# Optimization experiments

Hardware: AMD Instinct MI355X
Metric: run time of the kernel (lower is better)

## Reference

```python
import jax, jax.numpy as jnp
import numpy as np

N = 1024
H = 4096
W = 4096
K_COUNTS = 10
IOU_T = 0.5
NEG = -1e30  # -inf stand-in for unrecorded groups


def _box_iou(b):
    # b: [N,4] xyxy pixel coords -> [N,N] IoU (torchvision.ops.box_iou)
    area = (b[:, 2] - b[:, 0]) * (b[:, 3] - b[:, 1])
    ix1 = jnp.maximum(b[:, None, 0], b[None, :, 0])
    iy1 = jnp.maximum(b[:, None, 1], b[None, :, 1])
    ix2 = jnp.minimum(b[:, None, 2], b[None, :, 2])
    iy2 = jnp.minimum(b[:, None, 3], b[None, :, 3])
    inter = jnp.clip(ix2 - ix1, 0.0) * jnp.clip(iy2 - iy1, 0.0)
    return inter / (area[:, None] + area[None, :] - inter)


def _c_wsl(iou_gt, scores, counts):
    # Faithful vectorized c_wsl_fast: for every start box i, greedily sweep
    # j = i+1..N-1 adding boxes compatible (IoU <= T) with all current members;
    # when a group hits `counts` at the TOP of a j-iteration it is recorded
    # (check-before-add semantics, so a group completed at j = N-1 is never
    # recorded, matching the original break-based control flow). The final
    # answer is the LAST start achieving the max recorded score (>= update).
    n = scores.shape[0]
    starts = jnp.arange(n)
    carry0 = (
        jnp.eye(n, dtype=bool),            # sel[i, k]: box k in group of start i
        jnp.ones(n, jnp.int32),            # group sizes
        scores,                            # group scores
        jnp.zeros(n, bool),                # recorded flag (== break)
        jnp.full(n, NEG, scores.dtype),    # recorded score
        jnp.zeros((n, n), bool),           # recorded membership
    )

    def step(c, xs):
        j, sj, iou_j = xs  # iou_j = iou_gt[j] (> T bool row; matrix symmetric)
        sel, size, score, rec, rec_score, rec_sel = c
        active = (j > starts) & (~rec)
        do_rec = active & (size == counts)
        rec_sel = jnp.where(do_rec[:, None], sel, rec_sel)
        rec_score = jnp.where(do_rec, score, rec_score)
        rec = rec | do_rec
        compat = ~jnp.any(sel & iou_j[None, :], axis=1)
        add = active & (~do_rec) & (size < counts) & compat
        sel = sel.at[:, j].set(sel[:, j] | add)
        size = size + add.astype(size.dtype)
        score = score + jnp.where(add, sj, jnp.zeros((), score.dtype))
        return (sel, size, score, rec, rec_score, rec_sel), None

    (_, _, _, rec, rec_score, rec_sel), _ = jax.lax.scan(
        step, carry0, (starts, scores, iou_gt))
    masked = jnp.where(rec, rec_score, NEG)
    best = (n - 1) - jnp.argmax(masked[::-1])  # last argmax == '>=' update rule
    return jnp.where(jnp.any(rec), rec_sel[best], jnp.zeros(n, bool))


def reference(bbox, obj_scores, probs, counts):
    Hh, Ww = probs.shape
    # score_bbox_heatmap(reduction='mean'): mean of probs[y1:y2, x1:x2] per box,
    # computed exactly for all boxes with a zero-padded summed-area table.
    sat = jnp.pad(jnp.cumsum(jnp.cumsum(probs, axis=0), axis=1), ((1, 0), (1, 0)))
    x1 = jnp.clip(jnp.floor(bbox[:, 0]).astype(jnp.int32), 0, Ww)
    y1 = jnp.clip(jnp.floor(bbox[:, 1]).astype(jnp.int32), 0, Hh)
    x2 = jnp.clip(jnp.floor(bbox[:, 2]).astype(jnp.int32), 0, Ww)
    y2 = jnp.clip(jnp.floor(bbox[:, 3]).astype(jnp.int32), 0, Hh)
    sums = sat[y2, x2] - sat[y1, x2] - sat[y2, x1] + sat[y1, x1]
    cnt = jnp.maximum((y2 - y1) * (x2 - x1), 1).astype(probs.dtype)
    box_scores = sums / cnt
    # agg_score_method == 'mean'
    scores = 0.5 * (obj_scores + box_scores)
    # sort descending, then greedy IoU grouping on sorted boxes
    order = jnp.argsort(-scores)
    bbox_s = bbox[order]
    scores_s = scores[order]
    iou_gt = _box_iou(bbox_s) > IOU_T
    sel = _c_wsl(iou_gt, scores_s, counts)
    return scores_s * sel.astype(scores_s.dtype)


def setup_inputs() -> dict:
    key = jax.random.key(0)
    k1, k2, k3, k4, k5, k6 = jax.random.split(key, 6)
    cx = jax.random.uniform(k1, (N,), minval=0.15, maxval=0.85) * W
    cy = jax.random.uniform(k2, (N,), minval=0.15, maxval=0.85) * H
    bw = jnp.maximum(jax.random.uniform(k3, (N,), minval=0.02, maxval=0.25) * W, 8.0)
    bh = jnp.maximum(jax.random.uniform(k4, (N,), minval=0.02, maxval=0.25) * H, 8.0)
    bbox = jnp.stack([cx - bw / 2, cy - bh / 2, cx + bw / 2, cy + bh / 2], axis=1)
    obj_scores = jax.random.uniform(k5, (N,))
    probs = jax.random.uniform(k6, (H, W))
    return {"bbox": bbox, "obj_scores": obj_scores, "probs": probs, "counts": K_COUNTS}
```

## Files before the change

### kernel.cpp

```cpp
#include <hip/hip_runtime.h>

#define HH 4096
#define WW 4096
#define NB 1024
#define NCHUNK 256
#define CROWS 16
#define IOU_T 0.5f

typedef unsigned long long u64;

constexpr size_t OFF_PART   = 0;
constexpr size_t OFF_SC64   = OFF_PART   + (size_t)NCHUNK * WW * 8;
constexpr size_t OFF_ORDER  = OFF_SC64   + (size_t)NB * 8;
constexpr size_t OFF_CTR    = OFF_ORDER  + (size_t)NB * 4;
constexpr size_t OFF_IOU    = OFF_CTR    + 64;
constexpr size_t OFF_RECSC  = OFF_IOU    + (size_t)NB * 16 * 8;
constexpr size_t OFF_RECSEL = OFF_RECSC  + (size_t)NB * 8;
constexpr size_t OFF_CC     = OFF_RECSEL + (size_t)NB * 16 * 8;


__global__ void __launch_bounds__(256) k_stage(const float* __restrict__ probs,
        const float* __restrict__ bbox,
        double* __restrict__ part, float* __restrict__ Cc, int* __restrict__ ctr) {
    __shared__ int xlo_s[CROWS], xhi_s[CROWS];
    __shared__ int2 rng_s[CROWS];
    int tid = blockIdx.x * 256 + threadIdx.x;
    int c  = tid >> 10;
    int xq = tid & 1023;
    int t  = threadIdx.x;
    if (blockIdx.x == 0 && t == 0) *ctr = 0;
    if (t < CROWS) { xlo_s[t] = WW + 1; xhi_s[t] = -1; }
    __syncthreads();
    int r0 = c * CROWS;
    for (int i = t; i < NB; i += 256) {
        float4 bb = ((const float4*)bbox)[i];
        int x1 = min(max((int)floorf(bb.x), 0), WW);
        int y1 = min(max((int)floorf(bb.y), 0), HH);
        int x2 = min(max((int)floorf(bb.z), 0), WW);
        int y2 = min(max((int)floorf(bb.w), 0), HH);
        int ra = y1 - 1 - r0, rb = y2 - 1 - r0;
        if (ra >= 0 && ra < CROWS) { atomicMin(&xlo_s[ra], x1); atomicMax(&xhi_s[ra], x2); }
        if (rb >= 0 && rb < CROWS) { atomicMin(&xlo_s[rb], x1); atomicMax(&xhi_s[rb], x2); }
    }
    __syncthreads();
    if (t < CROWS) {
        int lo = xlo_s[t], hi = xhi_s[t];
        rng_s[t] = (hi >= 0) ? make_int2(lo >> 2, (hi + 3) >> 2) : make_int2(1, 0);
    }
    __syncthreads();
    const float4* p = (const float4*)probs + (size_t)r0 * (WW / 4) + xq;
    float4* Cc4 = (float4*)Cc;
    double a0 = 0.0, a1 = 0.0, a2 = 0.0, a3 = 0.0;
    for (int r = 0; r < CROWS; r += 8) {
        float4 q[8];
        #pragma unroll
        for (int k = 0; k < 8; k++) q[k] = p[(size_t)(r + k) * (WW / 4)];
        #pragma unroll
        for (int k = 0; k < 8; k++) {
            a0 += (double)q[k].x; a1 += (double)q[k].y;
            a2 += (double)q[k].z; a3 += (double)q[k].w;
            int2 d = rng_s[r + k];
            if (xq >= d.x && xq < d.y)
                Cc4[(size_t)(r0 + r + k) * (WW / 4) + xq] =
                    make_float4((float)a0, (float)a1, (float)a2, (float)a3);
        }
    }
    double2* pp = (double2*)(part + (size_t)c * WW) + xq * 2;
    pp[0] = make_double2(a0, a1);
    pp[1] = make_double2(a2, a3);
}

__global__ void k_chunkscan(double* __restrict__ part) {
    int x = blockIdx.x * blockDim.x + threadIdx.x;
    double carry = 0.0;
    for (int g = 0; g < NCHUNK / 16; g++) {
        double v[16];
        #pragma unroll
        for (int k = 0; k < 16; k++) v[k] = part[(size_t)(g * 16 + k) * WW + x];
        #pragma unroll
        for (int k = 0; k < 16; k++) { double tv = v[k]; v[k] = carry; carry += tv; }
        #pragma unroll
        for (int k = 0; k < 16; k++) part[(size_t)(g * 16 + k) * WW + x] = v[k];
    }
}

__global__ void __launch_bounds__(256) k_boxsum(const float* __restrict__ bbox,
                         const float* __restrict__ obj,
                         const float* __restrict__ Cc,
                         const double* __restrict__ part,
                         double* __restrict__ sc64) {
    int i = blockIdx.x;
    int t = threadIdx.x;
    float4 bb = ((const float4*)bbox)[i];
    int x1 = min(max((int)floorf(bb.x), 0), WW);
    int y1 = min(max((int)floorf(bb.y), 0), HH);
    int x2 = min(max((int)floorf(bb.z), 0), WW);
    int y2 = min(max((int)floorf(bb.w), 0), HH);
    bool h1 = (y1 >= 1), h2 = (y2 >= 1);
    const float*  r2 = Cc   + (size_t)(h2 ? (y2 - 1) : 0) * WW;
    const double* q2 = part + (size_t)(h2 ? ((y2 - 1) >> 4) : 0) * WW;
    const float*  r1 = Cc   + (size_t)(h1 ? (y1 - 1) : 0) * WW;
    const double* q1 = part + (size_t)(h1 ? ((y1 - 1) >> 4) : 0) * WW;
    double s = 0.0;
    for (int x = x1 + t; x < x2; x += 256) {
        double v2 = h2 ? ((double)r2[x] + q2[x]) : 0.0;
        double v1 = h1 ? ((double)r1[x] + q1[x]) : 0.0;
        s += (v2 - v1);
    }
    __shared__ double red[4];
    #pragma unroll
    for (int off = 32; off > 0; off >>= 1) s += __shfl_down(s, off);
    if ((t & 63) == 0) red[t >> 6] = s;
    __syncthreads();
    if (t == 0) {
        double tot = red[0] + red[1] + red[2] + red[3];
        long long cnt = (long long)(y2 - y1) * (long long)(x2 - x1);
        if (cnt < 1) cnt = 1;
        sc64[i] = 0.5 * ((double)obj[i] + tot / (double)cnt);
    }
}

__global__ void __launch_bounds__(128) k_rank(const double* __restrict__ sc64,
                                              int* __restrict__ order) {
    __shared__ double s[NB];
    int t = threadIdx.x;
    for (int k = t; k < NB; k += 128) s[k] = sc64[k];
    __syncthreads();
    int i = blockIdx.x * 128 + t;
    double si = s[i];
    int rank = 0;
    #pragma unroll 8
    for (int j = 0; j < NB; j++) {
        double sj = s[j];
        rank += (sj > si) || (sj == si && j < i);
    }
    order[rank] = i;
}

__global__ void k_iou(const int* __restrict__ order, const float* __restrict__ bbox,
                      u64* __restrict__ ioub) {
    int tid = blockIdx.x * blockDim.x + threadIdx.x;
    int i = tid >> 10;
    int j = tid & (NB - 1);
    float4 a = ((const float4*)bbox)[order[i]];
    float4 b = ((const float4*)bbox)[order[j]];
    float ai = (a.z - a.x) * (a.w - a.y);
    float aj = (b.z - b.x) * (b.w - b.y);
    float ix1 = fmaxf(a.x, b.x), iy1 = fmaxf(a.y, b.y);
    float ix2 = fminf(a.z, b.z), iy2 = fminf(a.w, b.w);
    float iw = fmaxf(ix2 - ix1, 0.0f), ih = fmaxf(iy2 - iy1, 0.0f);
    float inter = iw * ih;
    float iou_v = inter / (ai + aj - inter);
    bool bit = iou_v > IOU_T;
    u64 m = __ballot(bit);
    if ((threadIdx.x & 63) == 0) ioub[(size_t)i * 16 + (j >> 6)] = m;
}

__global__ void __launch_bounds__(64) k_group(const u64* __restrict__ ioub,
                        const int* __restrict__ order,
                        const double* __restrict__ sc64,
                        const int* __restrict__ counts,
                        double* __restrict__ recsc,
                        u64* __restrict__ recsel,
                        int* __restrict__ ctr,
                        float* __restrict__ out) {
    __shared__ double ssd_s[NB];
    __shared__ int lastflag;
    int t = threadIdx.x;
    int i = blockIdx.x * 64 + t;
    for (int k = t; k < NB; k += 64) ssd_s[k] = sc64[order[k]];
    __syncthreads();
    int K = counts[0];
    u64 inc[16], sel[16];
    int wi = i >> 6, bi = i & 63;
    #pragma unroll
    for (int w = 0; w < 16; w++) {
        inc[w] = ioub[(size_t)i * 16 + w];
        sel[w] = (w == wi) ? (1ULL << bi) : 0ULL;
    }
    int size = 1;
    double score = ssd_s[i];
    int last = i;
    #pragma unroll
    for (int w = 0; w < 16; w++) {
        if (w < wi || size >= K) continue;
        u64 avail = ~inc[w];
        if (w == wi) avail &= (bi == 63) ? 0ULL : (~0ULL << (bi + 1));
        while (avail != 0ULL && size < K) {
            int b = __builtin_ctzll(avail);
            int j = (w << 6) + b;
            sel[w] |= 1ULL << b;
            size++;
            score += ssd_s[j];
            last = j;
            const u64* rj = ioub + (size_t)j * 16;
            #pragma unroll
            for (int w2 = 0; w2 < 16; w2++) inc[w2] |= rj[w2];
            avail &= ~inc[w];
            avail &= ~(1ULL << b);
        }
    }
    int rec = (size == K) && (last < NB - 1);
    recsc[i] = rec ? score : -1e300;
    #pragma unroll
    for (int w = 0; w < 16; w++) recsel[(size_t)i * 16 + w] = sel[w];
    __threadfence();
    if (t == 0) lastflag = (atomicAdd(ctr, 1) == (int)gridDim.x - 1);
    __syncthreads();
    if (!lastflag) return;
    __threadfence();
    double bs = -1e301; int bidx = 0;
    for (int m = 0; m < 16; m++) {
        int k = t * 16 + m;
        double v = recsc[k];
        if (v >= bs) { bs = v; bidx = k; }
    }
    #pragma unroll
    for (int off = 32; off > 0; off >>= 1) {
        double ob = __shfl_down(bs, off);
        int oi = __shfl_down(bidx, off);
        if (ob > bs || (ob == bs && oi > bidx)) { bs = ob; bidx = oi; }
    }
    bs = __shfl(bs, 0);
    bidx = __shfl(bidx, 0);
    int any = bs > -1e299;
    for (int k = t; k < NB; k += 64) {
        float v = 0.0f;
        if (any && ((recsel[(size_t)bidx * 16 + (k >> 6)] >> (k & 63)) & 1ULL))
            v = (float)ssd_s[k];
        out[k] = v;
    }
}


extern "C" void kernel_launch(void* const* d_in, const int* in_sizes, int n_in,
                              void* d_out, int out_size, void* d_ws, size_t ws_size,
                              hipStream_t stream) {
    const float* bbox  = (const float*)d_in[0];
    const float* obj   = (const float*)d_in[1];
    const float* probs = (const float*)d_in[2];
    const int*   counts = (const int*)d_in[3];
    float* out = (float*)d_out;

    char* w = (char*)d_ws;
    double* part    = (double*)(w + OFF_PART);
    double* sc64    = (double*)(w + OFF_SC64);
    int*    order   = (int*)(w + OFF_ORDER);
    int*    ctr     = (int*)(w + OFF_CTR);
    u64*    ioub    = (u64*)(w + OFF_IOU);
    double* recsc   = (double*)(w + OFF_RECSC);
    u64*    recsel  = (u64*)(w + OFF_RECSEL);
    float*  Cc      = (float*)(w + OFF_CC);

    k_stage<<<(NCHUNK * WW / 4) / 256, 256, 0, stream>>>(probs, bbox, part, Cc, ctr);
    k_chunkscan<<<WW / 256, 256, 0, stream>>>(part);
    k_boxsum<<<NB, 256, 0, stream>>>(bbox, obj, Cc, part, sc64);
    k_rank<<<NB / 128, 128, 0, stream>>>(sc64, order);
    k_iou<<<(NB * NB) / 256, 256, 0, stream>>>(order, bbox, ioub);
    k_group<<<NB / 64, 64, 0, stream>>>(ioub, order, sc64, counts, recsc, recsel,
                                        ctr, out);
}
```

Measured before the change: 173.9 us.

## Fuse chunk scan into stage kernel and merge tail stages into one persistent kernel

The column chunk-scan now runs inside k_stage. The last 64 blocks to finish wait on an atomic counter until every stage block is done, then scan the columns. Box-sum, rank, IoU bitmask, grouping and final selection are merged into one 64-block kernel with software grid barriers in place of separate launches, and the launch count drops from six to two plus a memset. The cost is spin-waiting, reduced parallelism in the tail stages (64 blocks doing the IoU and box sums), and reliance on all 64 blocks being co-resident.

```diff
diff --git a/kernel.cpp b/kernel.cpp
--- a/kernel.cpp
+++ b/kernel.cpp
@@ -6,6 +6,8 @@
 #define NCHUNK 256
 #define CROWS 16
 #define IOU_T 0.5f
+#define NBLK_STAGE 1024
+#define NBLK_TAIL 64
 
 typedef unsigned long long u64;
 
@@ -18,17 +20,30 @@
 constexpr size_t OFF_RECSEL = OFF_RECSC  + (size_t)NB * 8;
 constexpr size_t OFF_CC     = OFF_RECSEL + (size_t)NB * 16 * 8;
 
+__device__ __forceinline__ void gbar(int* bctr, int round) {
+    __threadfence();
+    __syncthreads();
+    if (threadIdx.x == 0) {
+        __hip_atomic_fetch_add(bctr, 1, __ATOMIC_ACQ_REL, __HIP_MEMORY_SCOPE_AGENT);
+        while (__hip_atomic_load(bctr, __ATOMIC_ACQUIRE, __HIP_MEMORY_SCOPE_AGENT)
+               < NBLK_TAIL * round)
+            __builtin_amdgcn_s_sleep(2);
+    }
+    __syncthreads();
+    __threadfence();
+}
+
 
 __global__ void __launch_bounds__(256) k_stage(const float* __restrict__ probs,
         const float* __restrict__ bbox,
-        double* __restrict__ part, float* __restrict__ Cc, int* __restrict__ ctr) {
+        double* __restrict__ part, float* __restrict__ Cc, int* __restrict__ ctrs) {
     __shared__ int xlo_s[CROWS], xhi_s[CROWS];
     __shared__ int2 rng_s[CROWS];
+    __shared__ int sIdx;
     int tid = blockIdx.x * 256 + threadIdx.x;
     int c  = tid >> 10;
     int xq = tid & 1023;
     int t  = threadIdx.x;
-    if (blockIdx.x == 0 && t == 0) *ctr = 0;
     if (t < CROWS) { xlo_s[t] = WW + 1; xhi_s[t] = -1; }
     __syncthreads();
     int r0 = c * CROWS;
@@ -68,167 +83,193 @@
     double2* pp = (double2*)(part + (size_t)c * WW) + xq * 2;
     pp[0] = make_double2(a0, a1);
     pp[1] = make_double2(a2, a3);
+
+    __threadfence();
+    __syncthreads();
+    if (t == 0) sIdx = atomicAdd(&ctrs[0], 1);
+    __syncthreads();
+    int w = sIdx - (NBLK_STAGE - NBLK_TAIL);
+    if (w < 0) return;
+    if (t == 0) {
+        while (__hip_atomic_load(&ctrs[0], __ATOMIC_ACQUIRE, __HIP_MEMORY_SCOPE_AGENT)
+               < NBLK_STAGE)
+            __builtin_amdgcn_s_sleep(2);
+    }
+    __syncthreads();
+    __threadfence();
+    if (t < 64) {
+        int x = w * 64 + t;
+        double carry = 0.0;
+        for (int g = 0; g < NCHUNK / 16; g++) {
+            double v[16];
+            #pragma unroll
+            for (int k = 0; k < 16; k++) v[k] = part[(size_t)(g * 16 + k) * WW + x];
+            #pragma unroll
+            for (int k = 0; k < 16; k++) { double tv = v[k]; v[k] = carry; carry += tv; }
+            #pragma unroll
+            for (int k = 0; k < 16; k++) part[(size_t)(g * 16 + k) * WW + x] = v[k];
+        }
+    }
 }
 
-__global__ void k_chunkscan(double* __restrict__ part) {
-    int x = blockIdx.x * blockDim.x + threadIdx.x;
-    double carry = 0.0;
-    for (int g = 0; g < NCHUNK / 16; g++) {
-        double v[16];
+__global__ void __launch_bounds__(256) k_tail(const float* __restrict__ bbox,
+        const float* __restrict__ obj,
+        const float* __restrict__ Cc,
+        const double* __restrict__ part,
+        const int* __restrict__ counts,
+        double* __restrict__ sc64, int* __restrict__ order,
+        u64* __restrict__ ioub, double* __restrict__ recsc,
+        u64* __restrict__ recsel, int* __restrict__ ctrs,
+        float* __restrict__ out) {
+    __shared__ double s_sc[NB];
+    __shared__ int    ord_s[NB];
+    __shared__ float4 sbb[NB];
+    __shared__ int    rnk[16];
+    int b = blockIdx.x, t = threadIdx.x;
+    int* bctr = &ctrs[1];
+
+    {
+        int wv = t >> 6, l = t & 63;
+        for (int q = 0; q < 4; q++) {
+            int i = b * 16 + wv * 4 + q;
+            float4 bb = ((const float4*)bbox)[i];
+            int x1 = min(max((int)floorf(bb.x), 0), WW);
+            int y1 = min(max((int)floorf(bb.y), 0), HH);
+            int x2 = min(max((int)floorf(bb.z), 0), WW);
+            int y2 = min(max((int)floorf(bb.w), 0), HH);
+            bool h1 = (y1 >= 1), h2 = (y2 >= 1);
+            const float*  r2 = Cc   + (size_t)(h2 ? (y2 - 1) : 0) * WW;
+            const double* q2 = part + (size_t)(h2 ? ((y2 - 1) >> 4) : 0) * WW;
+            const float*  r1 = Cc   + (size_t)(h1 ? (y1 - 1) : 0) * WW;
+            const double* q1 = part + (size_t)(h1 ? ((y1 - 1) >> 4) : 0) * WW;
+            double s = 0.0;
+            for (int x = x1 + l; x < x2; x += 64) {
+                double v2 = h2 ? ((double)r2[x] + q2[x]) : 0.0;
+                double v1 = h1 ? ((double)r1[x] + q1[x]) : 0.0;
+                s += (v2 - v1);
+            }
+            #pragma unroll
+            for (int off = 32; off > 0; off >>= 1) s += __shfl_down(s, off);
+            if (l == 0) {
+                long long cnt = (long long)(y2 - y1) * (long long)(x2 - x1);
+                if (cnt < 1) cnt = 1;
+                sc64[i] = 0.5 * ((double)obj[i] + s / (double)cnt);
+            }
+        }
+    }
+    gbar(bctr, 1);
+
+    for (int k = t; k < NB; k += 256) s_sc[k] = sc64[k];
+    if (t < 16) rnk[t] = 0;
+    __syncthreads();
+    {
+        int q = t >> 4;
+        int g = t & 15;
+        int i = b * 16 + q;
+        double si = s_sc[i];
+        int p = 0;
+        for (int it = 0; it < 64; it++) {
+            int j = (g << 6) + ((it + 5 * g) & 63);
+            double sj = s_sc[j];
+            p += (sj > si) || (sj == si && j < i);
+        }
+        atomicAdd(&rnk[q], p);
+    }
+    __syncthreads();
+    if (t < 16) order[rnk[t]] = b * 16 + t;
+    gbar(bctr, 2);
+
+    for (int k = t; k < NB; k += 256) {
+        int o = order[k];
+        ord_s[k] = o;
+        sbb[k] = ((const float4*)bbox)[o];
+    }
+    __syncthreads();
+    {
+        int wv = t >> 6, l = t & 63;
+        for (int rr = 0; rr < 4; rr++) {
+            int i = b * 16 + wv * 4 + rr;
+            float4 a = sbb[i];
+            float ai = (a.z - a.x) * (a.w - a.y);
+            for (int wd = 0; wd < 16; wd++) {
+                float4 bb = sbb[(wd << 6) + l];
+                float aj = (bb.z - bb.x) * (bb.w - bb.y);
+                float ix1 = fmaxf(a.x, bb.x), iy1 = fmaxf(a.y, bb.y);
+                float ix2 = fminf(a.z, bb.z), iy2 = fminf(a.w, bb.w);
+                float iw = fmaxf(ix2 - ix1, 0.0f), ih = fmaxf(iy2 - iy1, 0.0f);
+                float inter = iw * ih;
+                float iou_v = inter / (ai + aj - inter);
+                u64 m = __ballot(iou_v > IOU_T);
+                if (l == 0) ioub[(size_t)i * 16 + wd] = m;
+            }
+        }
+    }
+    gbar(bctr, 3);
+
+    {
+        int K = counts[0];
+        if (t < 16) {
+            int i = b * 16 + t;
+            u64 inc[16], sel[16];
+            int wi = i >> 6, bi = i & 63;
+            #pragma unroll
+            for (int w = 0; w < 16; w++) {
+                inc[w] = ioub[(size_t)i * 16 + w];
+                sel[w] = (w == wi) ? (1ULL << bi) : 0ULL;
+            }
+            int size = 1;
+            double score = s_sc[ord_s[i]];
+            int last = i;
+            #pragma unroll
+            for (int w = 0; w < 16; w++) {
+                if (w < wi || size >= K) continue;
+                u64 avail = ~inc[w];
+                if (w == wi) avail &= (bi == 63) ? 0ULL : (~0ULL << (bi + 1));
+                while (avail != 0ULL && size < K) {
+                    int bj = __builtin_ctzll(avail);
+                    int j = (w << 6) + bj;
+                    sel[w] |= 1ULL << bj;
+                    size++;
+                    score += s_sc[ord_s[j]];
+                    last = j;
+                    const u64* rj = ioub + (size_t)j * 16;
+                    #pragma unroll
+                    for (int w2 = 0; w2 < 16; w2++) inc[w2] |= rj[w2];
+                    avail &= ~inc[w];
+                    avail &= ~(1ULL << bj);
+                }
+            }
+            int rec = (size == K) && (last < NB - 1);
+            recsc[i] = rec ? score : -1e300;
+            #pragma unroll
+            for (int w = 0; w < 16; w++) recsel[(size_t)i * 16 + w] = sel[w];
+        }
+    }
+    gbar(bctr, 4);
+    if (b != 0) return;
+
+    if (t < 64) {
+        double bs = -1e301; int bidx = 0;
+        for (int m = 0; m < 16; m++) {
+            int k = t * 16 + m;
+            double v = recsc[k];
+            if (v >= bs) { bs = v; bidx = k; }
+        }
         #pragma unroll
-        for (int k = 0; k < 16; k++) v[k] = part[(size_t)(g * 16 + k) * WW + x];
-        #pragma unroll
-        for (int k = 0; k < 16; k++) { double tv = v[k]; v[k] = carry; carry += tv; }
-        #pragma unroll
-        for (int k = 0; k < 16; k++) part[(size_t)(g * 16 + k) * WW + x] = v[k];
-    }
-}
-
-__global__ void __launch_bounds__(256) k_boxsum(const float* __restrict__ bbox,
-                         const float* __restrict__ obj,
-                         const float* __restrict__ Cc,
-                         const double* __restrict__ part,
-                         double* __restrict__ sc64) {
-    int i = blockIdx.x;
-    int t = threadIdx.x;
-    float4 bb = ((const float4*)bbox)[i];
-    int x1 = min(max((int)floorf(bb.x), 0), WW);
-    int y1 = min(max((int)floorf(bb.y), 0), HH);
-    int x2 = min(max((int)floorf(bb.z), 0), WW);
-    int y2 = min(max((int)floorf(bb.w), 0), HH);
-    bool h1 = (y1 >= 1), h2 = (y2 >= 1);
-    const float*  r2 = Cc   + (size_t)(h2 ? (y2 - 1) : 0) * WW;
-    const double* q2 = part + (size_t)(h2 ? ((y2 - 1) >> 4) : 0) * WW;
-    const float*  r1 = Cc   + (size_t)(h1 ? (y1 - 1) : 0) * WW;
-    const double* q1 = part + (size_t)(h1 ? ((y1 - 1) >> 4) : 0) * WW;
-    double s = 0.0;
-    for (int x = x1 + t; x < x2; x += 256) {
-        double v2 = h2 ? ((double)r2[x] + q2[x]) : 0.0;
-        double v1 = h1 ? ((double)r1[x] + q1[x]) : 0.0;
-        s += (v2 - v1);
-    }
-    __shared__ double red[4];
-    #pragma unroll
-    for (int off = 32; off > 0; off >>= 1) s += __shfl_down(s, off);
-    if ((t & 63) == 0) red[t >> 6] = s;
-    __syncthreads();
-    if (t == 0) {
-        double tot = red[0] + red[1] + red[2] + red[3];
-        long long cnt = (long long)(y2 - y1) * (long long)(x2 - x1);
-        if (cnt < 1) cnt = 1;
-        sc64[i] = 0.5 * ((double)obj[i] + tot / (double)cnt);
-    }
-}
-
-__global__ void __launch_bounds__(128) k_rank(const double* __restrict__ sc64,
-                                              int* __restrict__ order) {
-    __shared__ double s[NB];
-    int t = threadIdx.x;
-    for (int k = t; k < NB; k += 128) s[k] = sc64[k];
-    __syncthreads();
-    int i = blockIdx.x * 128 + t;
-    double si = s[i];
-    int rank = 0;
-    #pragma unroll 8
-    for (int j = 0; j < NB; j++) {
-        double sj = s[j];
-        rank += (sj > si) || (sj == si && j < i);
-    }
-    order[rank] = i;
-}
-
-__global__ void k_iou(const int* __restrict__ order, const float* __restrict__ bbox,
-                      u64* __restrict__ ioub) {
-    int tid = blockIdx.x * blockDim.x + threadIdx.x;
-    int i = tid >> 10;
-    int j = tid & (NB - 1);
-    float4 a = ((const float4*)bbox)[order[i]];
-    float4 b = ((const float4*)bbox)[order[j]];
-    float ai = (a.z - a.x) * (a.w - a.y);
-    float aj = (b.z - b.x) * (b.w - b.y);
-    float ix1 = fmaxf(a.x, b.x), iy1 = fmaxf(a.y, b.y);
-    float ix2 = fminf(a.z, b.z), iy2 = fminf(a.w, b.w);
-    float iw = fmaxf(ix2 - ix1, 0.0f), ih = fmaxf(iy2 - iy1, 0.0f);
-    float inter = iw * ih;
-    float iou_v = inter / (ai + aj - inter);
-    bool bit = iou_v > IOU_T;
-    u64 m = __ballot(bit);
-    if ((threadIdx.x & 63) == 0) ioub[(size_t)i * 16 + (j >> 6)] = m;
-}
-
-__global__ void __launch_bounds__(64) k_group(const u64* __restrict__ ioub,
-                        const int* __restrict__ order,
-                        const double* __restrict__ sc64,
-                        const int* __restrict__ counts,
-                        double* __restrict__ recsc,
-                        u64* __restrict__ recsel,
-                        int* __restrict__ ctr,
-                        float* __restrict__ out) {
-    __shared__ double ssd_s[NB];
-    __shared__ int lastflag;
-    int t = threadIdx.x;
-    int i = blockIdx.x * 64 + t;
-    for (int k = t; k < NB; k += 64) ssd_s[k] = sc64[order[k]];
-    __syncthreads();
-    int K = counts[0];
-    u64 inc[16], sel[16];
-    int wi = i >> 6, bi = i & 63;
-    #pragma unroll
-    for (int w = 0; w < 16; w++) {
-        inc[w] = ioub[(size_t)i * 16 + w];
-        sel[w] = (w == wi) ? (1ULL << bi) : 0ULL;
-    }
-    int size = 1;
-    double score = ssd_s[i];
-    int last = i;
-    #pragma unroll
-    for (int w = 0; w < 16; w++) {
-        if (w < wi || size >= K) continue;
-        u64 avail = ~inc[w];
-        if (w == wi) avail &= (bi == 63) ? 0ULL : (~0ULL << (bi + 1));
-        while (avail != 0ULL && size < K) {
-            int b = __builtin_ctzll(avail);
-            int j = (w << 6) + b;
-            sel[w] |= 1ULL << b;
-            size++;
-            score += ssd_s[j];
-            last = j;
-            const u64* rj = ioub + (size_t)j * 16;
-            #pragma unroll
-            for (int w2 = 0; w2 < 16; w2++) inc[w2] |= rj[w2];
-            avail &= ~inc[w];
-            avail &= ~(1ULL << b);
-        }
-    }
-    int rec = (size == K) && (last < NB - 1);
-    recsc[i] = rec ? score : -1e300;
-    #pragma unroll
-    for (int w = 0; w < 16; w++) recsel[(size_t)i * 16 + w] = sel[w];
-    __threadfence();
-    if (t == 0) lastflag = (atomicAdd(ctr, 1) == (int)gridDim.x - 1);
-    __syncthreads();
-    if (!lastflag) return;
-    __threadfence();
-    double bs = -1e301; int bidx = 0;
-    for (int m = 0; m < 16; m++) {
-        int k = t * 16 + m;
-        double v = recsc[k];
-        if (v >= bs) { bs = v; bidx = k; }
-    }
-    #pragma unroll
-    for (int off = 32; off > 0; off >>= 1) {
-        double ob = __shfl_down(bs, off);
-        int oi = __shfl_down(bidx, off);
-        if (ob > bs || (ob == bs && oi > bidx)) { bs = ob; bidx = oi; }
-    }
-    bs = __shfl(bs, 0);
-    bidx = __shfl(bidx, 0);
-    int any = bs > -1e299;
-    for (int k = t; k < NB; k += 64) {
-        float v = 0.0f;
-        if (any && ((recsel[(size_t)bidx * 16 + (k >> 6)] >> (k & 63)) & 1ULL))
-            v = (float)ssd_s[k];
-        out[k] = v;
+        for (int off = 32; off > 0; off >>= 1) {
+            double ob = __shfl_down(bs, off);
+            int oi = __shfl_down(bidx, off);
+            if (ob > bs || (ob == bs && oi > bidx)) { bs = ob; bidx = oi; }
+        }
+        bs = __shfl(bs, 0);
+        bidx = __shfl(bidx, 0);
+        int any = bs > -1e299;
+        for (int k = t; k < NB; k += 64) {
+            float v = 0.0f;
+            if (any && ((recsel[(size_t)bidx * 16 + (k >> 6)] >> (k & 63)) & 1ULL))
+                v = (float)s_sc[ord_s[k]];
+            out[k] = v;
+        }
     }
 }
 
@@ -246,17 +287,15 @@
     double* part    = (double*)(w + OFF_PART);
     double* sc64    = (double*)(w + OFF_SC64);
     int*    order   = (int*)(w + OFF_ORDER);
-    int*    ctr     = (int*)(w + OFF_CTR);
+    int*    ctrs    = (int*)(w + OFF_CTR);
     u64*    ioub    = (u64*)(w + OFF_IOU);
     double* recsc   = (double*)(w + OFF_RECSC);
     u64*    recsel  = (u64*)(w + OFF_RECSEL);
     float*  Cc      = (float*)(w + OFF_CC);
 
-    k_stage<<<(NCHUNK * WW / 4) / 256, 256, 0, stream>>>(probs, bbox, part, Cc, ctr);
-    k_chunkscan<<<WW / 256, 256, 0, stream>>>(part);
-    k_boxsum<<<NB, 256, 0, stream>>>(bbox, obj, Cc, part, sc64);
-    k_rank<<<NB / 128, 128, 0, stream>>>(sc64, order);
-    k_iou<<<(NB * NB) / 256, 256, 0, stream>>>(order, bbox, ioub);
-    k_group<<<NB / 64, 64, 0, stream>>>(ioub, order, sc64, counts, recsc, recsel,
-                                        ctr, out);
+    hipMemsetAsync(w + OFF_CTR, 0, 64, stream);
+    k_stage<<<NBLK_STAGE, 256, 0, stream>>>(probs, bbox, part, Cc, ctrs);
+    k_tail<<<NBLK_TAIL, 256, 0, stream>>>(bbox, obj, Cc, part, counts,
+                                          sc64, order, ioub, recsc, recsel,
+                                          ctrs, out);
 }
```

After: 387.6 us. 2.23x slower.
